# Kernel optimization log

Measured on AMD Instinct MI355X. Metric: run time of the kernel, lower is better.

## Reference

```python
import jax, jax.numpy as jnp
import numpy as np

T_STEPS = 100
T_EMB = 16
EPS = 1e-8


def sin_emb(t, dim):
    # sinusoidal_time_embedding: [cos(t*f), sin(t*f)] with f = exp(-log(1e4)*i/half)
    half = dim // 2
    freqs = jnp.exp(-jnp.log(jnp.float32(10000.0)) * jnp.arange(half, dtype=jnp.float32) / half)
    a = t.astype(jnp.float32)[:, None] * freqs[None, :]
    return jnp.concatenate([jnp.cos(a), jnp.sin(a)], axis=-1)


def lstm_layer(x_tbf, W_ih, W_hh, b):
    # x_tbf: [T, B, F]; torch gate order i, f, g, o
    B = x_tbf.shape[1]
    H = W_hh.shape[1]

    def step(carry, x_t):
        h, c = carry
        g = x_t @ W_ih.T + h @ W_hh.T + b
        i, f, gg, o = jnp.split(g, 4, axis=-1)
        c = jax.nn.sigmoid(f) * c + jax.nn.sigmoid(i) * jnp.tanh(gg)
        h = jax.nn.sigmoid(o) * jnp.tanh(c)
        return (h, c), h

    z = jnp.zeros((B, H), x_tbf.dtype)
    (h, c), ys = jax.lax.scan(step, (z, z), x_tbf)
    return ys, h


def _forward(x_hist, x_future, y0, turb_idx, pred_steps, init_noise, turb_emb,
             W_ih0, W_hh0, b_ih0, b_hh0, W_ih1, W_hh1, b_ih1, b_hh1,
             W1, b1, W2, b2, W3, b3):
    betas = jnp.linspace(1e-4, 0.02, T_STEPS).astype(jnp.float32)
    alphas = 1.0 - betas
    alpha_bars = jnp.cumprod(alphas)

    B = x_hist.shape[0]
    emb = turb_emb[turb_idx]  # [B, E]
    eh = jnp.broadcast_to(emb[:, None, :], (B, x_hist.shape[1], emb.shape[1]))
    ef = jnp.broadcast_to(emb[:, None, :], (B, x_future.shape[1], emb.shape[1]))
    xh = jnp.concatenate([x_hist, eh], axis=-1).transpose(1, 0, 2)    # [T_in, B, F+E]
    xf = jnp.concatenate([x_future, ef], axis=-1).transpose(1, 0, 2)  # [P, B, exo+E]

    ys0, _ = lstm_layer(xh, W_ih0, W_hh0, b_ih0 + b_hh0)
    _, enc_out = lstm_layer(ys0, W_ih1, W_hh1, b_ih1 + b_hh1)         # [B, H] = h[-1]

    def mlp(x):
        h = jax.nn.relu(x @ W1.T + b1)
        h = jax.nn.relu(h @ W2.T + b2)
        return h @ W3.T + b3

    def ar_step(prev_y, xs):
        exo_t, step, y_init = xs
        cond = jnp.concatenate([enc_out, exo_t, prev_y], axis=1)  # [B, cond_dim]
        h_e = sin_emb(jnp.full((B,), step), T_EMB)

        def dstep(y, t):
            t_e = sin_emb(jnp.full((B,), t), T_EMB)
            eps_hat = mlp(jnp.concatenate([cond, y, t_e, h_e], axis=1))  # [B,1]
            b_t, a_t, ab_t = betas[t], alphas[t], alpha_bars[t]
            pred_x0 = (y - jnp.sqrt(1.0 - ab_t) * eps_hat) / (jnp.sqrt(ab_t) + EPS)
            mean = (y - b_t / (jnp.sqrt(1.0 - ab_t) + EPS) * eps_hat) / (jnp.sqrt(a_t) + EPS)
            # eval mode -> deterministic sampling: posterior noise term is zero
            return jnp.where(t == 0, pred_x0, mean), None

        y, _ = jax.lax.scan(dstep, y_init, jnp.arange(T_STEPS - 1, -1, -1))
        return y, y[:, 0]

    _, seq = jax.lax.scan(ar_step, y0, (xf, jnp.arange(pred_steps), init_noise))
    return seq.T[:, :, None]  # [B, pred_steps, 1]


def setup_inputs() -> dict:
    key = jax.random.key(0)
    ks = list(jax.random.split(key, 24))
    kit = iter(ks)
    B, T_IN, F_IN, EXO, EMB, PRED, HID, NTURB = 1024, 96, 8, 6, 16, 8, 128, 100
    in0 = F_IN + EMB                 # 24
    cond_dim = HID + EXO + EMB + 1   # 151
    in_mlp = cond_dim + 1 + T_EMB + T_EMB  # 184

    def nrm(shape, s=0.05):
        return jax.random.normal(next(kit), shape, jnp.float32) * s

    return {
        'x_hist': jax.random.normal(next(kit), (B, T_IN, F_IN), jnp.float32),
        'x_future': jax.random.normal(next(kit), (B, PRED, EXO), jnp.float32),
        'y0': jnp.zeros((B, 1), jnp.float32),
        'turb_idx': jax.random.randint(next(kit), (B,), 0, NTURB),
        'pred_steps': PRED,
        'init_noise': jax.random.normal(next(kit), (PRED, B, 1), jnp.float32),
        'turb_emb': nrm((NTURB, EMB), 0.1),
        'W_ih0': nrm((4 * HID, in0)), 'W_hh0': nrm((4 * HID, HID)),
        'b_ih0': jnp.zeros((4 * HID,), jnp.float32), 'b_hh0': jnp.zeros((4 * HID,), jnp.float32),
        'W_ih1': nrm((4 * HID, HID)), 'W_hh1': nrm((4 * HID, HID)),
        'b_ih1': jnp.zeros((4 * HID,), jnp.float32), 'b_hh1': jnp.zeros((4 * HID,), jnp.float32),
        'W1': nrm((HID, in_mlp)), 'b1': jnp.zeros((HID,), jnp.float32),
        'W2': nrm((HID, HID)), 'b2': jnp.zeros((HID,), jnp.float32),
        'W3': nrm((1, HID)), 'b3': jnp.zeros((1,), jnp.float32),
    }


def reference(x_hist, x_future, y0, turb_idx, pred_steps, init_noise, turb_emb,
              W_ih0, W_hh0, b_ih0, b_hh0, W_ih1, W_hh1, b_ih1, b_hh1,
              W1, b1, W2, b2, W3, b3):
    return _forward(x_hist, x_future, y0, turb_idx, pred_steps, init_noise, turb_emb,
                    W_ih0, W_hh0, b_ih0, b_hh0, W_ih1, W_hh1, b_ih1, b_hh1,
                    W1, b1, W2, b2, W3, b3)
```

## Files before the change

kernel.cpp:

```cpp
#include <hip/hip_runtime.h>
#include <hip/hip_fp16.h>
#include <stdint.h>


typedef __attribute__((ext_vector_type(2))) _Float16 half2_t;
typedef __attribute__((ext_vector_type(8))) _Float16 v8h;
typedef __attribute__((ext_vector_type(4))) float v4f;

#define DEV __device__ __forceinline__

DEV uint32_t pack2f(float a, float b) {
  __half ha = __float2half_rn(a), hb = __float2half_rn(b);
  return (uint32_t)__half_as_ushort(ha) | ((uint32_t)__half_as_ushort(hb) << 16);
}

DEV float2 up2(uint32_t u) {
  half2_t h = __builtin_bit_cast(half2_t, u);
  return make_float2((float)h.x, (float)h.y);
}

DEV float fast_ex2(float x) {
#if __has_builtin(__builtin_amdgcn_exp2f)
  return __builtin_amdgcn_exp2f(x);
#else
  return exp2f(x);
#endif
}
DEV float fast_rcp(float x) {
#if __has_builtin(__builtin_amdgcn_rcpf)
  return __builtin_amdgcn_rcpf(x);
#else
  return 1.f / x;
#endif
}
DEV float sigm(float x) { return fast_rcp(1.f + fast_ex2(-1.4426950408889634f * x)); }
DEV float tanh_f(float x) {
  return 2.f * fast_rcp(1.f + fast_ex2(-2.8853900817779268f * x)) - 1.f;
}

DEV uint32_t pk_add(uint32_t a, uint32_t b) {
  return __builtin_bit_cast(uint32_t,
      __builtin_bit_cast(half2_t, a) + __builtin_bit_cast(half2_t, b));
}

DEV uint32_t pk_relufma(uint32_t w, uint32_t y, uint32_t b) {
  half2_t r = __builtin_bit_cast(half2_t, w) * __builtin_bit_cast(half2_t, y) +
              __builtin_bit_cast(half2_t, b);
  half2_t z = {(_Float16)0.f, (_Float16)0.f};
#if __has_builtin(__builtin_elementwise_max)
  r = __builtin_elementwise_max(r, z);
#else
  uint32_t u = __builtin_bit_cast(uint32_t, r);
  uint32_t mask = ((u >> 15) & 1u) * 0xFFFFu | ((u >> 31) & 1u) * 0xFFFF0000u;
  r = __builtin_bit_cast(half2_t, u & ~mask);
#endif
  return __builtin_bit_cast(uint32_t, r);
}

DEV uint32_t cvtpk(float y) {
#if __has_builtin(__builtin_amdgcn_cvt_pkrtz)
  return __builtin_bit_cast(uint32_t, __builtin_amdgcn_cvt_pkrtz(y, y));
#else
  return pack2f(y, y);
#endif
}

DEV float rowsum16(float v) {
  int x;
  x = __builtin_amdgcn_update_dpp(0, __builtin_bit_cast(int, v), 0x111, 0xf, 0xf, true);
  v += __builtin_bit_cast(float, x);
  x = __builtin_amdgcn_update_dpp(0, __builtin_bit_cast(int, v), 0x112, 0xf, 0xf, true);
  v += __builtin_bit_cast(float, x);
  x = __builtin_amdgcn_update_dpp(0, __builtin_bit_cast(int, v), 0x114, 0xf, 0xf, true);
  v += __builtin_bit_cast(float, x);
  x = __builtin_amdgcn_update_dpp(0, __builtin_bit_cast(int, v), 0x118, 0xf, 0xf, true);
  v += __builtin_bit_cast(float, x);
  return v;
}

static constexpr size_t OFF_XH  = 0;
static constexpr size_t OFF_W0  = 4718592;
static constexpr size_t OFF_BS0 = 4882432;
static constexpr size_t OFF_W1L = 4884480;
static constexpr size_t OFF_BS1 = 5146624;
static constexpr size_t OFF_W2P = 5148672;
static constexpr size_t OFF_ENC = 5181440;
static constexpr size_t OFF_YS0 = 5705728;

__global__ void k_prep_xh(const float* __restrict__ xh, const int* __restrict__ tix,
                          const float* __restrict__ temb, uint32_t* __restrict__ out) {
  int idx = blockIdx.x * 256 + threadIdx.x;
  if (idx >= 96 * 1024 * 12) return;
  int m = idx % 12;
  int tb = idx / 12;
  int b = tb & 1023, t = tb >> 10;
  int k0 = 2 * m, k1 = k0 + 1;
  float v0 = (k0 < 8) ? xh[(b * 96 + t) * 8 + k0] : temb[tix[b] * 16 + (k0 - 8)];
  float v1 = (k1 < 8) ? xh[(b * 96 + t) * 8 + k1] : temb[tix[b] * 16 + (k1 - 8)];
  out[idx] = pack2f(v0, v1);
}

__global__ void k_prep_w(const float* __restrict__ Wih0, const float* __restrict__ Whh0,
                         const float* __restrict__ bih0, const float* __restrict__ bhh0,
                         const float* __restrict__ Wih1, const float* __restrict__ Whh1,
                         const float* __restrict__ bih1, const float* __restrict__ bhh1,
                         const float* __restrict__ W2,
                         uint32_t* __restrict__ w0p, uint32_t* __restrict__ w1p,
                         uint32_t* __restrict__ w2p, float* __restrict__ bs0,
                         float* __restrict__ bs1) {
  int idx = blockIdx.x * 256 + threadIdx.x;
  if (idx < 40960) {
    int w = idx / 5120;
    int r = idx % 5120;
    int T = r / 1280; r %= 1280;
    int f = r / 256;  r %= 256;
    int l = r >> 2, c = r & 3;
    int m = l & 15, qf = l >> 4;
    int g = (m & 3) * 128 + w * 16 + (m >> 2) * 4 + T;
    int k0 = f * 32 + qf * 8 + 2 * c, k1 = k0 + 1;
    float a = (k0 < 24) ? Wih0[g * 24 + k0] : ((k0 < 152) ? Whh0[g * 128 + k0 - 24] : 0.f);
    float b = (k1 < 24) ? Wih0[g * 24 + k1] : ((k1 < 152) ? Whh0[g * 128 + k1 - 24] : 0.f);
    w0p[idx] = pack2f(a, b);
  } else if (idx < 106496) {
    int i = idx - 40960;
    int w = i / 8192;
    int r = i % 8192;
    int T = r / 2048; r %= 2048;
    int f = r / 256;  r %= 256;
    int l = r >> 2, c = r & 3;
    int m = l & 15, qf = l >> 4;
    int g = (m & 3) * 128 + w * 16 + (m >> 2) * 4 + T;
    int k0 = f * 32 + qf * 8 + 2 * c, k1 = k0 + 1;
    float a = (k0 < 128) ? Wih1[g * 128 + k0] : Whh1[g * 128 + k0 - 128];
    float b = (k1 < 128) ? Wih1[g * 128 + k1] : Whh1[g * 128 + k1 - 128];
    w1p[i] = pack2f(a, b);
  } else if (idx < 114688) {
    int i = idx - 106496;
    w2p[i] = pack2f(W2[2 * i], W2[2 * i + 1]);
  } else if (idx < 115200) {
    int i = idx - 114688;
    bs0[i] = bih0[i] + bhh0[i];
  } else if (idx < 115712) {
    int i = idx - 115200;
    bs1[i] = bih1[i] + bhh1[i];
  }
}

__global__ __launch_bounds__(512, 2) void k_lstm0(const uint32_t* __restrict__ xh16,
                                                  const uint32_t* __restrict__ w0A,
                                                  const float* __restrict__ bs0,
                                                  __half* __restrict__ ys0) {
  __shared__ __align__(16) __half inb[2][16][160];
  const int tid = threadIdx.x;
  const int w = tid >> 6, l = tid & 63;
  const int n = l & 15, ql = l >> 4;
  const int ju = w * 16 + ql * 4;
  const int bbase = blockIdx.x * 16;

  uint4 Af[4][5];
#pragma unroll
  for (int T = 0; T < 4; T++)
#pragma unroll
    for (int f = 0; f < 5; f++)
      Af[T][f] = ((const uint4*)w0A)[((w * 4 + T) * 5 + f) * 64 + l];
  float bias[4][4];
#pragma unroll
  for (int T = 0; T < 4; T++)
#pragma unroll
    for (int r = 0; r < 4; r++) bias[T][r] = bs0[r * 128 + ju + T];

  for (int i = tid; i < 2560; i += 512) ((uint32_t*)inb)[i] = 0u;
  __syncthreads();
  if (tid < 192) {
    int b = tid / 12, m = tid % 12;
    ((uint32_t*)&inb[0][b][0])[m] = xh16[(0 * 1024 + bbase + b) * 12 + m];
  }
  float cst[4] = {0.f, 0.f, 0.f, 0.f};
  __syncthreads();

  for (int t = 0; t < 96; t++) {
    const int cur = t & 1, nxt = cur ^ 1;
    uint32_t sx = 0;
    int sb = 0, sm = 0;
    if (t < 95 && tid < 192) {
      sb = tid / 12; sm = tid % 12;
      sx = xh16[((t + 1) * 1024 + bbase + sb) * 12 + sm];
    }
    v4f acc[4];
#pragma unroll
    for (int T = 0; T < 4; T++) acc[T] = (v4f){0.f, 0.f, 0.f, 0.f};
#pragma unroll
    for (int f = 0; f < 5; f++) {
      uint4 bu = *(const uint4*)&inb[cur][n][f * 32 + ql * 8];
      v8h Bv = __builtin_bit_cast(v8h, bu);
#pragma unroll
      for (int T = 0; T < 4; T++)
        acc[T] = __builtin_amdgcn_mfma_f32_16x16x32_f16(
            __builtin_bit_cast(v8h, Af[T][f]), Bv, acc[T], 0, 0, 0);
    }
    float hv[4];
#pragma unroll
    for (int T = 0; T < 4; T++) {
      float gi = acc[T][0] + bias[T][0];
      float gf = acc[T][1] + bias[T][1];
      float gg = acc[T][2] + bias[T][2];
      float go = acc[T][3] + bias[T][3];
      float c = sigm(gf) * cst[T] + sigm(gi) * tanh_f(gg);
      cst[T] = c;
      hv[T] = sigm(go) * tanh_f(c);
    }
    uint32_t h01 = pack2f(hv[0], hv[1]), h23 = pack2f(hv[2], hv[3]);
    *(uint2*)&inb[nxt][n][24 + ju] = make_uint2(h01, h23);
    *(uint2*)((__half*)ys0 + (size_t)(t * 1024 + bbase + n) * 128 + ju) = make_uint2(h01, h23);
    if (t < 95 && tid < 192) ((uint32_t*)&inb[nxt][sb][0])[sm] = sx;
    __syncthreads();
  }
}

__global__ __launch_bounds__(512, 2) void k_lstm1(const uint32_t* __restrict__ ys0u,
                                                  const uint32_t* __restrict__ w1A,
                                                  const float* __restrict__ bs1,
                                                  float* __restrict__ enc) {
  __shared__ __align__(16) __half inb[2][16][264];
  const int tid = threadIdx.x;
  const int w = tid >> 6, l = tid & 63;
  const int n = l & 15, ql = l >> 4;
  const int ju = w * 16 + ql * 4;
  const int bbase = blockIdx.x * 16;
  const int sb = tid >> 5, sc = tid & 31;

  uint4 Af[4][8];
#pragma unroll
  for (int T = 0; T < 4; T++)
#pragma unroll
    for (int f = 0; f < 8; f++)
      Af[T][f] = ((const uint4*)w1A)[((w * 4 + T) * 8 + f) * 64 + l];
  float bias[4][4];
#pragma unroll
  for (int T = 0; T < 4; T++)
#pragma unroll
    for (int r = 0; r < 4; r++) bias[T][r] = bs1[r * 128 + ju + T];

  for (int i = tid; i < 4224; i += 512) ((uint32_t*)inb)[i] = 0u;
  __syncthreads();
  {
    uint2 v = ((const uint2*)ys0u)[(size_t)(0 * 1024 + bbase + sb) * 32 + sc];
    *(uint2*)&inb[0][sb][sc * 4] = v;
  }
  float cst[4] = {0.f, 0.f, 0.f, 0.f};
  __syncthreads();

  for (int t = 0; t < 96; t++) {
    const int cur = t & 1, nxt = cur ^ 1;
    uint2 sv = make_uint2(0u, 0u);
    if (t < 95)
      sv = ((const uint2*)ys0u)[(size_t)((t + 1) * 1024 + bbase + sb) * 32 + sc];
    v4f acc[4];
#pragma unroll
    for (int T = 0; T < 4; T++) acc[T] = (v4f){0.f, 0.f, 0.f, 0.f};
#pragma unroll
    for (int f = 0; f < 8; f++) {
      uint4 bu = *(const uint4*)&inb[cur][n][f * 32 + ql * 8];
      v8h Bv = __builtin_bit_cast(v8h, bu);
#pragma unroll
      for (int T = 0; T < 4; T++)
        acc[T] = __builtin_amdgcn_mfma_f32_16x16x32_f16(
            __builtin_bit_cast(v8h, Af[T][f]), Bv, acc[T], 0, 0, 0);
    }
    float hv[4];
#pragma unroll
    for (int T = 0; T < 4; T++) {
      float gi = acc[T][0] + bias[T][0];
      float gf = acc[T][1] + bias[T][1];
      float gg = acc[T][2] + bias[T][2];
      float go = acc[T][3] + bias[T][3];
      float c = sigm(gf) * cst[T] + sigm(gi) * tanh_f(gg);
      cst[T] = c;
      hv[T] = sigm(go) * tanh_f(c);
    }
    *(uint2*)&inb[nxt][n][128 + ju] = make_uint2(pack2f(hv[0], hv[1]), pack2f(hv[2], hv[3]));
    if (t < 95) *(uint2*)&inb[nxt][sb][sc * 4] = sv;
    if (t == 95)
      *(float4*)&enc[(size_t)(bbase + n) * 128 + ju] = make_float4(hv[0], hv[1], hv[2], hv[3]);
    __syncthreads();
  }
}

__global__ __launch_bounds__(256, 1) void k_diff(
    const float* __restrict__ xfut, const float* __restrict__ y0,
    const int* __restrict__ tix, const float* __restrict__ noise,
    const float* __restrict__ temb, const float* __restrict__ W1,
    const float* __restrict__ b1, const float* __restrict__ b2,
    const float* __restrict__ W3, const float* __restrict__ b3,
    const uint32_t* __restrict__ w2p, const float* __restrict__ enc,
    float* __restrict__ out) {
  __shared__ uint32_t W1sL[128 * 65];
  __shared__ uint32_t W1xL[128 * 29];
  __shared__ uint32_t encPL[16 * 65];
  __shared__ uint32_t embPL[16 * 9];
  __shared__ float teL[100][16];
  __shared__ float2 ccL[100];
  __shared__ __align__(16) __half tprojL[100 * 128];
  __shared__ __half hprojL[8 * 128];
  __shared__ __align__(16) float partL[2][4][16];
  __shared__ uint32_t encdL[256 * 17];

  const int tid = threadIdx.x;
  const int w = tid >> 6, l = tid & 63;
  const int m = l & 15, q = l >> 4;
  const int bbase = blockIdx.x * 16;

  for (int i = tid; i < 128 * 64; i += 256) {
    int r = i >> 6, c = i & 63;
    W1sL[r * 65 + c] = pack2f(W1[r * 184 + 2 * c], W1[r * 184 + 2 * c + 1]);
  }
  for (int i = tid; i < 128 * 28; i += 256) {
    int r = i / 28, c = i % 28;
    W1xL[r * 29 + c] = pack2f(W1[r * 184 + 128 + 2 * c], W1[r * 184 + 129 + 2 * c]);
  }
  for (int i = tid; i < 16 * 64; i += 256) {
    int bb = i >> 6, c = i & 63;
    encPL[bb * 65 + c] = pack2f(enc[(bbase + bb) * 128 + 2 * c],
                                enc[(bbase + bb) * 128 + 2 * c + 1]);
  }
  for (int i = tid; i < 16 * 8; i += 256) {
    int bb = i >> 3, c = i & 7;
    const float* er = temb + tix[bbase + bb] * 16;
    embPL[bb * 9 + c] = pack2f(er[2 * c], er[2 * c + 1]);
  }
  for (int p = tid; p < 1600; p += 256) {
    int tt = p >> 4, i = p & 15;
    float f = expf(-logf(10000.f) * (float)(i & 7) / 8.f);
    float a = (float)tt * f;
    teL[tt][i] = (i < 8) ? cosf(a) : sinf(a);
  }
  for (int qq = tid; qq < 100; qq += 256) {
    float ab = 1.f, beta = 0.f;
    for (int i = 0; i <= qq; i++) {
      beta = 1e-4f + (0.02f - 1e-4f) * (float)i / 99.f;
      ab *= (1.f - beta);
    }
    float cs, cd;
    if (qq == 0) { cs = sqrtf(1.f - ab); cd = 1.f / (sqrtf(ab) + 1e-8f); }
    else { cs = beta / (sqrtf(1.f - ab) + 1e-8f); cd = 1.f / (sqrtf(1.f - beta) + 1e-8f); }
    ccL[qq] = make_float2(cs, cd);
  }
  __syncthreads();

  {
    int k = tid & 127, hs = tid >> 7;
    float wte[16], whe[16];
#pragma unroll
    for (int i = 0; i < 8; i++) {
      float2 a = up2(W1xL[k * 29 + 12 + i]);
      wte[2 * i] = a.x; wte[2 * i + 1] = a.y;
      float2 bqq = up2(W1xL[k * 29 + 20 + i]);
      whe[2 * i] = bqq.x; whe[2 * i + 1] = bqq.y;
    }
    for (int tt = hs * 50; tt < hs * 50 + 50; tt++) {
      float s = 0.f;
#pragma unroll
      for (int i = 0; i < 16; i++) s += wte[i] * teL[tt][i];
      tprojL[tt * 128 + k] = __float2half_rn(s);
    }
    if (hs == 0) {
      for (int ss = 0; ss < 8; ss++) {
        float s = 0.f;
#pragma unroll
        for (int i = 0; i < 16; i++) s += whe[i] * teL[ss][i];
        hprojL[ss * 128 + k] = __float2half_rn(s);
      }
    }
  }

  for (int pi = 0; pi < 16; pi++) {
    int k0 = (pi >> 2) * 32 + q * 8 + (pi & 3) * 2;
    half2_t a0 = {(_Float16)0.f, (_Float16)0.f};
    half2_t a1 = a0;
    const uint32_t* wr0 = &W1sL[k0 * 65];
    const uint32_t* wr1 = &W1sL[(k0 + 1) * 65];
    const uint32_t* ep = &encPL[m * 65];
#pragma unroll 8
    for (int c = 0; c < 64; c++) {
      half2_t e = __builtin_bit_cast(half2_t, ep[c]);
      a0 += __builtin_bit_cast(half2_t, wr0[c]) * e;
      a1 += __builtin_bit_cast(half2_t, wr1[c]) * e;
    }
#pragma unroll
    for (int c = 0; c < 8; c++) {
      half2_t e = __builtin_bit_cast(half2_t, embPL[m * 9 + c]);
      a0 += __builtin_bit_cast(half2_t, W1xL[k0 * 29 + 3 + c]) * e;
      a1 += __builtin_bit_cast(half2_t, W1xL[(k0 + 1) * 29 + 3 + c]) * e;
    }
    float e0 = b1[k0] + (float)a0.x + (float)a0.y;
    float e1 = b1[k0 + 1] + (float)a1.x + (float)a1.y;
    encdL[tid * 17 + pi] = pack2f(e0, e1);
  }

  uint4 Bf[2][4];
  const uint4* w2u4 = (const uint4*)w2p;
#pragma unroll
  for (int tt = 0; tt < 2; tt++) {
    int n = w * 32 + tt * 16 + m;
#pragma unroll
    for (int f = 0; f < 4; f++) Bf[tt][f] = w2u4[n * 16 + f * 4 + q];
  }
  const float w3v0 = W3[w * 32 + m], w3v1 = W3[w * 32 + 16 + m];
  const float b2v0 = b2[w * 32 + m], b2v1 = b2[w * 32 + 16 + m];
  const float b3v = b3[0];

  uint32_t w1yP[16];
#pragma unroll
  for (int pi = 0; pi < 16; pi++) {
    int k0 = (pi >> 2) * 32 + q * 8 + (pi & 3) * 2;
    uint32_t ua = W1xL[k0 * 29 + 11];
    uint32_t ub = W1xL[(k0 + 1) * 29 + 11];
    w1yP[pi] = (ua >> 16) | (ub & 0xFFFF0000u);
  }

  float prev_y = y0[bbase + m];
  float noi[8];
#pragma unroll
  for (int s = 0; s < 8; s++) noi[s] = noise[s * 1024 + bbase + m];
  __syncthreads();

  int buf = 0;
  for (int s = 0; s < 8; s++) {
    float xf[6];
#pragma unroll
    for (int i = 0; i < 6; i++) xf[i] = xfut[((bbase + m) * 8 + s) * 6 + i];
    uint32_t bph[16];
#pragma unroll
    for (int pi = 0; pi < 16; pi++) {
      int k0 = (pi >> 2) * 32 + q * 8 + (pi & 3) * 2;
      float2 ed = up2(encdL[tid * 17 + pi]);
      float e0 = ed.x, e1 = ed.y;
#pragma unroll
      for (int c = 0; c < 3; c++) {
        float2 w0v = up2(W1xL[k0 * 29 + c]);
        float2 w1v = up2(W1xL[(k0 + 1) * 29 + c]);
        e0 += w0v.x * xf[2 * c] + w0v.y * xf[2 * c + 1];
        e1 += w1v.x * xf[2 * c] + w1v.y * xf[2 * c + 1];
      }
      e0 += up2(W1xL[k0 * 29 + 11]).x * prev_y;
      e1 += up2(W1xL[(k0 + 1) * 29 + 11]).x * prev_y;
      e0 += (float)hprojL[s * 128 + k0];
      e1 += (float)hprojL[s * 128 + k0 + 1];
      bph[pi] = pack2f(e0, e1);
    }

    float y = noi[s];
    uint32_t bt[16];
    {
      const uint4* tb = (const uint4*)(tprojL + 99 * 128 + q * 8);
      uint4 t0 = tb[0], t1 = tb[4], t2 = tb[8], t3 = tb[12];
      bt[0] = pk_add(bph[0], t0.x);  bt[1] = pk_add(bph[1], t0.y);
      bt[2] = pk_add(bph[2], t0.z);  bt[3] = pk_add(bph[3], t0.w);
      bt[4] = pk_add(bph[4], t1.x);  bt[5] = pk_add(bph[5], t1.y);
      bt[6] = pk_add(bph[6], t1.z);  bt[7] = pk_add(bph[7], t1.w);
      bt[8] = pk_add(bph[8], t2.x);  bt[9] = pk_add(bph[9], t2.y);
      bt[10] = pk_add(bph[10], t2.z); bt[11] = pk_add(bph[11], t2.w);
      bt[12] = pk_add(bph[12], t3.x); bt[13] = pk_add(bph[13], t3.y);
      bt[14] = pk_add(bph[14], t3.z); bt[15] = pk_add(bph[15], t3.w);
    }
    float2 ccv = ccL[99];

    for (int t = 99; t >= 0; t--) {
      uint32_t yP = cvtpk(y);
      v4f c0a = {0.f, 0.f, 0.f, 0.f}, c0b = c0a, c1a = c0a, c1b = c0a;
#pragma unroll
      for (int f = 0; f < 4; f++) {
        uint4 au;
        au.x = pk_relufma(w1yP[4 * f + 0], yP, bt[4 * f + 0]);
        au.y = pk_relufma(w1yP[4 * f + 1], yP, bt[4 * f + 1]);
        au.z = pk_relufma(w1yP[4 * f + 2], yP, bt[4 * f + 2]);
        au.w = pk_relufma(w1yP[4 * f + 3], yP, bt[4 * f + 3]);
        v8h A = __builtin_bit_cast(v8h, au);
        if (f & 1) {
          c0b = __builtin_amdgcn_mfma_f32_16x16x32_f16(A, __builtin_bit_cast(v8h, Bf[0][f]), c0b, 0, 0, 0);
          c1b = __builtin_amdgcn_mfma_f32_16x16x32_f16(A, __builtin_bit_cast(v8h, Bf[1][f]), c1b, 0, 0, 0);
        } else {
          c0a = __builtin_amdgcn_mfma_f32_16x16x32_f16(A, __builtin_bit_cast(v8h, Bf[0][f]), c0a, 0, 0, 0);
          c1a = __builtin_amdgcn_mfma_f32_16x16x32_f16(A, __builtin_bit_cast(v8h, Bf[1][f]), c1a, 0, 0, 0);
        }
      }
      const int tn = (t > 0) ? t - 1 : 0;
      const uint4* tb = (const uint4*)(tprojL + tn * 128 + q * 8);
      uint4 t0 = tb[0], t1 = tb[4], t2 = tb[8], t3 = tb[12];
      float2 ccn = ccL[tn];
      v4f c0 = c0a + c0b, c1 = c1a + c1b;
      float pr[4];
#pragma unroll
      for (int r = 0; r < 4; r++) {
        pr[r] = fmaxf(c0[r] + b2v0, 0.f) * w3v0 + fmaxf(c1[r] + b2v1, 0.f) * w3v1;
        pr[r] = rowsum16(pr[r]);
      }
      if ((l & 15) == 15)
        *(float4*)&partL[buf][w][q * 4] = make_float4(pr[0], pr[1], pr[2], pr[3]);
      uint32_t btn[16];
      btn[0] = pk_add(bph[0], t0.x);  btn[1] = pk_add(bph[1], t0.y);
      btn[2] = pk_add(bph[2], t0.z);  btn[3] = pk_add(bph[3], t0.w);
      btn[4] = pk_add(bph[4], t1.x);  btn[5] = pk_add(bph[5], t1.y);
      btn[6] = pk_add(bph[6], t1.z);  btn[7] = pk_add(bph[7], t1.w);
      btn[8] = pk_add(bph[8], t2.x);  btn[9] = pk_add(bph[9], t2.y);
      btn[10] = pk_add(bph[10], t2.z); btn[11] = pk_add(bph[11], t2.w);
      btn[12] = pk_add(bph[12], t3.x); btn[13] = pk_add(bph[13], t3.y);
      btn[14] = pk_add(bph[14], t3.z); btn[15] = pk_add(bph[15], t3.w);
      __syncthreads();
      float eps = b3v + ((partL[buf][0][m] + partL[buf][1][m]) +
                         (partL[buf][2][m] + partL[buf][3][m]));
      y = (y - ccv.x * eps) * ccv.y;
      ccv = ccn;
#pragma unroll
      for (int pi = 0; pi < 16; pi++) bt[pi] = btn[pi];
      buf ^= 1;
    }
    if (w == 0 && l < 16) out[(bbase + l) * 8 + s] = y;
    prev_y = y;
  }
}

extern "C" void kernel_launch(void* const* d_in, const int* in_sizes, int n_in,
                              void* d_out, int out_size, void* d_ws, size_t ws_size,
                              hipStream_t stream) {
  const float* x_hist    = (const float*)d_in[0];
  const float* x_future  = (const float*)d_in[1];
  const float* y0        = (const float*)d_in[2];
  const int*   turb_idx  = (const int*)d_in[3];
  const float* init_noise = (const float*)d_in[5];
  const float* turb_emb  = (const float*)d_in[6];
  const float* W_ih0     = (const float*)d_in[7];
  const float* W_hh0     = (const float*)d_in[8];
  const float* b_ih0     = (const float*)d_in[9];
  const float* b_hh0     = (const float*)d_in[10];
  const float* W_ih1     = (const float*)d_in[11];
  const float* W_hh1     = (const float*)d_in[12];
  const float* b_ih1     = (const float*)d_in[13];
  const float* b_hh1     = (const float*)d_in[14];
  const float* W1        = (const float*)d_in[15];
  const float* b1        = (const float*)d_in[16];
  const float* W2        = (const float*)d_in[17];
  const float* b2        = (const float*)d_in[18];
  const float* W3        = (const float*)d_in[19];
  const float* b3        = (const float*)d_in[20];

  char* ws = (char*)d_ws;
  uint32_t* xh16 = (uint32_t*)(ws + OFF_XH);
  uint32_t* w0p  = (uint32_t*)(ws + OFF_W0);
  float*    bs0  = (float*)(ws + OFF_BS0);
  uint32_t* w1p  = (uint32_t*)(ws + OFF_W1L);
  float*    bs1  = (float*)(ws + OFF_BS1);
  uint32_t* w2p  = (uint32_t*)(ws + OFF_W2P);
  float*    encf = (float*)(ws + OFF_ENC);
  __half*   ys0h = (__half*)(ws + OFF_YS0);

  k_prep_xh<<<4608, 256, 0, stream>>>(x_hist, turb_idx, turb_emb, xh16);
  k_prep_w<<<452, 256, 0, stream>>>(W_ih0, W_hh0, b_ih0, b_hh0,
                                    W_ih1, W_hh1, b_ih1, b_hh1,
                                    W2, w0p, w1p, w2p, bs0, bs1);
  k_lstm0<<<64, 512, 0, stream>>>(xh16, w0p, bs0, ys0h);
  k_lstm1<<<64, 512, 0, stream>>>((const uint32_t*)ys0h, w1p, bs1, encf);
  k_diff<<<64, 256, 0, stream>>>(x_future, y0, turb_idx, init_noise, turb_emb,
                                 W1, b1, b2, W3, b3, w2p, encf, (float*)d_out);
}
```

Before: 675.7 us.

## Process two 16-row batch chunks per diffusion block and use lighter LDS barriers

The diffusion kernel now handles 32 batch rows per block as two interleaved 16-row chains, halving the grid to 32 blocks. Each denoising step issues independent MFMA chains for both chunks, so one chunk's dependency latency can be hidden behind the other's work, and the per-step barrier cost is spread over twice the rows. The LSTM and diffusion barriers are replaced by an inline s_waitcnt lgkmcnt(0) plus s_barrier that waits only on LDS traffic. In exchange, fewer CUs are used, register pressure roughly doubles in the diffusion loop, and the weight-staging prologue is repeated over fewer blocks but each block does more of it.

After: 928.1 us. 37.4% more time.

```diff
diff --git a/kernel.cpp b/kernel.cpp
--- a/kernel.cpp
+++ b/kernel.cpp
@@ -8,6 +8,10 @@
 typedef __attribute__((ext_vector_type(4))) float v4f;
 
 #define DEV __device__ __forceinline__
+
+DEV void barrier_lds() {
+  asm volatile("s_waitcnt lgkmcnt(0)\ns_barrier" ::: "memory");
+}
 
 DEV uint32_t pack2f(float a, float b) {
   __half ha = __float2half_rn(a), hb = __float2half_rn(b);
@@ -213,7 +217,7 @@
     *(uint2*)&inb[nxt][n][24 + ju] = make_uint2(h01, h23);
     *(uint2*)((__half*)ys0 + (size_t)(t * 1024 + bbase + n) * 128 + ju) = make_uint2(h01, h23);
     if (t < 95 && tid < 192) ((uint32_t*)&inb[nxt][sb][0])[sm] = sx;
-    __syncthreads();
+    barrier_lds();
   }
 }
 
@@ -282,7 +286,7 @@
     if (t < 95) *(uint2*)&inb[nxt][sb][sc * 4] = sv;
     if (t == 95)
       *(float4*)&enc[(size_t)(bbase + n) * 128 + ju] = make_float4(hv[0], hv[1], hv[2], hv[3]);
-    __syncthreads();
+    barrier_lds();
   }
 }
 
@@ -296,19 +300,19 @@
     float* __restrict__ out) {
   __shared__ uint32_t W1sL[128 * 65];
   __shared__ uint32_t W1xL[128 * 29];
-  __shared__ uint32_t encPL[16 * 65];
-  __shared__ uint32_t embPL[16 * 9];
+  __shared__ uint32_t encPL[32 * 65];
+  __shared__ uint32_t embPL[32 * 9];
   __shared__ float teL[100][16];
   __shared__ float2 ccL[100];
   __shared__ __align__(16) __half tprojL[100 * 128];
   __shared__ __half hprojL[8 * 128];
-  __shared__ __align__(16) float partL[2][4][16];
-  __shared__ uint32_t encdL[256 * 17];
+  __shared__ __align__(16) float partL[2][2][4][16];
+  __shared__ uint32_t encdL[2][256 * 17];
 
   const int tid = threadIdx.x;
   const int w = tid >> 6, l = tid & 63;
   const int m = l & 15, q = l >> 4;
-  const int bbase = blockIdx.x * 16;
+  const int bbase = blockIdx.x * 32;
 
   for (int i = tid; i < 128 * 64; i += 256) {
     int r = i >> 6, c = i & 63;
@@ -318,12 +322,12 @@
     int r = i / 28, c = i % 28;
     W1xL[r * 29 + c] = pack2f(W1[r * 184 + 128 + 2 * c], W1[r * 184 + 129 + 2 * c]);
   }
-  for (int i = tid; i < 16 * 64; i += 256) {
+  for (int i = tid; i < 32 * 64; i += 256) {
     int bb = i >> 6, c = i & 63;
     encPL[bb * 65 + c] = pack2f(enc[(bbase + bb) * 128 + 2 * c],
                                 enc[(bbase + bb) * 128 + 2 * c + 1]);
   }
-  for (int i = tid; i < 16 * 8; i += 256) {
+  for (int i = tid; i < 32 * 8; i += 256) {
     int bb = i >> 3, c = i & 7;
     const float* er = temb + tix[bbase + bb] * 16;
     embPL[bb * 9 + c] = pack2f(er[2 * c], er[2 * c + 1]);
@@ -373,28 +377,31 @@
     }
   }
 
-  for (int pi = 0; pi < 16; pi++) {
-    int k0 = (pi >> 2) * 32 + q * 8 + (pi & 3) * 2;
-    half2_t a0 = {(_Float16)0.f, (_Float16)0.f};
-    half2_t a1 = a0;
-    const uint32_t* wr0 = &W1sL[k0 * 65];
-    const uint32_t* wr1 = &W1sL[(k0 + 1) * 65];
-    const uint32_t* ep = &encPL[m * 65];
+#pragma unroll
+  for (int ch = 0; ch < 2; ch++) {
+    for (int pi = 0; pi < 16; pi++) {
+      int k0 = (pi >> 2) * 32 + q * 8 + (pi & 3) * 2;
+      half2_t a0 = {(_Float16)0.f, (_Float16)0.f};
+      half2_t a1 = a0;
+      const uint32_t* wr0 = &W1sL[k0 * 65];
+      const uint32_t* wr1 = &W1sL[(k0 + 1) * 65];
+      const uint32_t* ep = &encPL[(ch * 16 + m) * 65];
 #pragma unroll 8
-    for (int c = 0; c < 64; c++) {
-      half2_t e = __builtin_bit_cast(half2_t, ep[c]);
-      a0 += __builtin_bit_cast(half2_t, wr0[c]) * e;
-      a1 += __builtin_bit_cast(half2_t, wr1[c]) * e;
-    }
-#pragma unroll
-    for (int c = 0; c < 8; c++) {
-      half2_t e = __builtin_bit_cast(half2_t, embPL[m * 9 + c]);
-      a0 += __builtin_bit_cast(half2_t, W1xL[k0 * 29 + 3 + c]) * e;
-      a1 += __builtin_bit_cast(half2_t, W1xL[(k0 + 1) * 29 + 3 + c]) * e;
-    }
-    float e0 = b1[k0] + (float)a0.x + (float)a0.y;
-    float e1 = b1[k0 + 1] + (float)a1.x + (float)a1.y;
-    encdL[tid * 17 + pi] = pack2f(e0, e1);
+      for (int c = 0; c < 64; c++) {
+        half2_t e = __builtin_bit_cast(half2_t, ep[c]);
+        a0 += __builtin_bit_cast(half2_t, wr0[c]) * e;
+        a1 += __builtin_bit_cast(half2_t, wr1[c]) * e;
+      }
+#pragma unroll
+      for (int c = 0; c < 8; c++) {
+        half2_t e = __builtin_bit_cast(half2_t, embPL[(ch * 16 + m) * 9 + c]);
+        a0 += __builtin_bit_cast(half2_t, W1xL[k0 * 29 + 3 + c]) * e;
+        a1 += __builtin_bit_cast(half2_t, W1xL[(k0 + 1) * 29 + 3 + c]) * e;
+      }
+      float e0 = b1[k0] + (float)a0.x + (float)a0.y;
+      float e1 = b1[k0 + 1] + (float)a1.x + (float)a1.y;
+      encdL[ch][tid * 17 + pi] = pack2f(e0, e1);
+    }
   }
 
   uint4 Bf[2][4];
@@ -418,105 +425,121 @@
     w1yP[pi] = (ua >> 16) | (ub & 0xFFFF0000u);
   }
 
-  float prev_y = y0[bbase + m];
-  float noi[8];
-#pragma unroll
-  for (int s = 0; s < 8; s++) noi[s] = noise[s * 1024 + bbase + m];
+  float py0 = y0[bbase + m], py1 = y0[bbase + 16 + m];
   __syncthreads();
 
   int buf = 0;
   for (int s = 0; s < 8; s++) {
-    float xf[6];
-#pragma unroll
-    for (int i = 0; i < 6; i++) xf[i] = xfut[((bbase + m) * 8 + s) * 6 + i];
-    uint32_t bph[16];
+    float xf0[6], xf1[6];
+#pragma unroll
+    for (int i = 0; i < 6; i++) {
+      xf0[i] = xfut[((bbase + m) * 8 + s) * 6 + i];
+      xf1[i] = xfut[((bbase + 16 + m) * 8 + s) * 6 + i];
+    }
+    uint32_t bph0[16], bph1[16];
 #pragma unroll
     for (int pi = 0; pi < 16; pi++) {
       int k0 = (pi >> 2) * 32 + q * 8 + (pi & 3) * 2;
-      float2 ed = up2(encdL[tid * 17 + pi]);
-      float e0 = ed.x, e1 = ed.y;
+      float2 ed0 = up2(encdL[0][tid * 17 + pi]);
+      float2 ed1 = up2(encdL[1][tid * 17 + pi]);
+      float e00 = ed0.x, e01 = ed0.y, e10 = ed1.x, e11 = ed1.y;
 #pragma unroll
       for (int c = 0; c < 3; c++) {
         float2 w0v = up2(W1xL[k0 * 29 + c]);
         float2 w1v = up2(W1xL[(k0 + 1) * 29 + c]);
-        e0 += w0v.x * xf[2 * c] + w0v.y * xf[2 * c + 1];
-        e1 += w1v.x * xf[2 * c] + w1v.y * xf[2 * c + 1];
-      }
-      e0 += up2(W1xL[k0 * 29 + 11]).x * prev_y;
-      e1 += up2(W1xL[(k0 + 1) * 29 + 11]).x * prev_y;
-      e0 += (float)hprojL[s * 128 + k0];
-      e1 += (float)hprojL[s * 128 + k0 + 1];
-      bph[pi] = pack2f(e0, e1);
-    }
-
-    float y = noi[s];
-    uint32_t bt[16];
+        e00 += w0v.x * xf0[2 * c] + w0v.y * xf0[2 * c + 1];
+        e01 += w1v.x * xf0[2 * c] + w1v.y * xf0[2 * c + 1];
+        e10 += w0v.x * xf1[2 * c] + w0v.y * xf1[2 * c + 1];
+        e11 += w1v.x * xf1[2 * c] + w1v.y * xf1[2 * c + 1];
+      }
+      float wp0 = up2(W1xL[k0 * 29 + 11]).x;
+      float wp1 = up2(W1xL[(k0 + 1) * 29 + 11]).x;
+      e00 += wp0 * py0;  e01 += wp1 * py0;
+      e10 += wp0 * py1;  e11 += wp1 * py1;
+      float hp0 = (float)hprojL[s * 128 + k0];
+      float hp1 = (float)hprojL[s * 128 + k0 + 1];
+      bph0[pi] = pack2f(e00 + hp0, e01 + hp1);
+      bph1[pi] = pack2f(e10 + hp0, e11 + hp1);
+    }
+
+    float ya = noise[s * 1024 + bbase + m];
+    float yb = noise[s * 1024 + bbase + 16 + m];
+    uint32_t bt0[16], bt1[16];
     {
       const uint4* tb = (const uint4*)(tprojL + 99 * 128 + q * 8);
       uint4 t0 = tb[0], t1 = tb[4], t2 = tb[8], t3 = tb[12];
-      bt[0] = pk_add(bph[0], t0.x);  bt[1] = pk_add(bph[1], t0.y);
-      bt[2] = pk_add(bph[2], t0.z);  bt[3] = pk_add(bph[3], t0.w);
-      bt[4] = pk_add(bph[4], t1.x);  bt[5] = pk_add(bph[5], t1.y);
-      bt[6] = pk_add(bph[6], t1.z);  bt[7] = pk_add(bph[7], t1.w);
-      bt[8] = pk_add(bph[8], t2.x);  bt[9] = pk_add(bph[9], t2.y);
-      bt[10] = pk_add(bph[10], t2.z); bt[11] = pk_add(bph[11], t2.w);
-      bt[12] = pk_add(bph[12], t3.x); bt[13] = pk_add(bph[13], t3.y);
-      bt[14] = pk_add(bph[14], t3.z); bt[15] = pk_add(bph[15], t3.w);
+      uint32_t tv[16] = {t0.x, t0.y, t0.z, t0.w, t1.x, t1.y, t1.z, t1.w,
+                         t2.x, t2.y, t2.z, t2.w, t3.x, t3.y, t3.z, t3.w};
+#pragma unroll
+      for (int pi = 0; pi < 16; pi++) {
+        bt0[pi] = pk_add(bph0[pi], tv[pi]);
+        bt1[pi] = pk_add(bph1[pi], tv[pi]);
+      }
     }
     float2 ccv = ccL[99];
 
     for (int t = 99; t >= 0; t--) {
-      uint32_t yP = cvtpk(y);
-      v4f c0a = {0.f, 0.f, 0.f, 0.f}, c0b = c0a, c1a = c0a, c1b = c0a;
+      uint32_t yPa = cvtpk(ya), yPb = cvtpk(yb);
+      v4f d00 = {0.f, 0.f, 0.f, 0.f}, d01 = d00, d10 = d00, d11 = d00;
 #pragma unroll
       for (int f = 0; f < 4; f++) {
         uint4 au;
-        au.x = pk_relufma(w1yP[4 * f + 0], yP, bt[4 * f + 0]);
-        au.y = pk_relufma(w1yP[4 * f + 1], yP, bt[4 * f + 1]);
-        au.z = pk_relufma(w1yP[4 * f + 2], yP, bt[4 * f + 2]);
-        au.w = pk_relufma(w1yP[4 * f + 3], yP, bt[4 * f + 3]);
+        au.x = pk_relufma(w1yP[4 * f + 0], yPa, bt0[4 * f + 0]);
+        au.y = pk_relufma(w1yP[4 * f + 1], yPa, bt0[4 * f + 1]);
+        au.z = pk_relufma(w1yP[4 * f + 2], yPa, bt0[4 * f + 2]);
+        au.w = pk_relufma(w1yP[4 * f + 3], yPa, bt0[4 * f + 3]);
         v8h A = __builtin_bit_cast(v8h, au);
-        if (f & 1) {
-          c0b = __builtin_amdgcn_mfma_f32_16x16x32_f16(A, __builtin_bit_cast(v8h, Bf[0][f]), c0b, 0, 0, 0);
-          c1b = __builtin_amdgcn_mfma_f32_16x16x32_f16(A, __builtin_bit_cast(v8h, Bf[1][f]), c1b, 0, 0, 0);
-        } else {
-          c0a = __builtin_amdgcn_mfma_f32_16x16x32_f16(A, __builtin_bit_cast(v8h, Bf[0][f]), c0a, 0, 0, 0);
-          c1a = __builtin_amdgcn_mfma_f32_16x16x32_f16(A, __builtin_bit_cast(v8h, Bf[1][f]), c1a, 0, 0, 0);
-        }
+        d00 = __builtin_amdgcn_mfma_f32_16x16x32_f16(A, __builtin_bit_cast(v8h, Bf[0][f]), d00, 0, 0, 0);
+        d01 = __builtin_amdgcn_mfma_f32_16x16x32_f16(A, __builtin_bit_cast(v8h, Bf[1][f]), d01, 0, 0, 0);
+        uint4 av;
+        av.x = pk_relufma(w1yP[4 * f + 0], yPb, bt1[4 * f + 0]);
+        av.y = pk_relufma(w1yP[4 * f + 1], yPb, bt1[4 * f + 1]);
+        av.z = pk_relufma(w1yP[4 * f + 2], yPb, bt1[4 * f + 2]);
+        av.w = pk_relufma(w1yP[4 * f + 3], yPb, bt1[4 * f + 3]);
+        v8h Ab = __builtin_bit_cast(v8h, av);
+        d10 = __builtin_amdgcn_mfma_f32_16x16x32_f16(Ab, __builtin_bit_cast(v8h, Bf[0][f]), d10, 0, 0, 0);
+        d11 = __builtin_amdgcn_mfma_f32_16x16x32_f16(Ab, __builtin_bit_cast(v8h, Bf[1][f]), d11, 0, 0, 0);
       }
       const int tn = (t > 0) ? t - 1 : 0;
       const uint4* tb = (const uint4*)(tprojL + tn * 128 + q * 8);
       uint4 t0 = tb[0], t1 = tb[4], t2 = tb[8], t3 = tb[12];
       float2 ccn = ccL[tn];
-      v4f c0 = c0a + c0b, c1 = c1a + c1b;
-      float pr[4];
+      float pra[4], prb[4];
 #pragma unroll
       for (int r = 0; r < 4; r++) {
-        pr[r] = fmaxf(c0[r] + b2v0, 0.f) * w3v0 + fmaxf(c1[r] + b2v1, 0.f) * w3v1;
-        pr[r] = rowsum16(pr[r]);
-      }
-      if ((l & 15) == 15)
-        *(float4*)&partL[buf][w][q * 4] = make_float4(pr[0], pr[1], pr[2], pr[3]);
-      uint32_t btn[16];
-      btn[0] = pk_add(bph[0], t0.x);  btn[1] = pk_add(bph[1], t0.y);
-      btn[2] = pk_add(bph[2], t0.z);  btn[3] = pk_add(bph[3], t0.w);
-      btn[4] = pk_add(bph[4], t1.x);  btn[5] = pk_add(bph[5], t1.y);
-      btn[6] = pk_add(bph[6], t1.z);  btn[7] = pk_add(bph[7], t1.w);
-      btn[8] = pk_add(bph[8], t2.x);  btn[9] = pk_add(bph[9], t2.y);
-      btn[10] = pk_add(bph[10], t2.z); btn[11] = pk_add(bph[11], t2.w);
-      btn[12] = pk_add(bph[12], t3.x); btn[13] = pk_add(bph[13], t3.y);
-      btn[14] = pk_add(bph[14], t3.z); btn[15] = pk_add(bph[15], t3.w);
-      __syncthreads();
-      float eps = b3v + ((partL[buf][0][m] + partL[buf][1][m]) +
-                         (partL[buf][2][m] + partL[buf][3][m]));
-      y = (y - ccv.x * eps) * ccv.y;
+        pra[r] = fmaxf(d00[r] + b2v0, 0.f) * w3v0 + fmaxf(d01[r] + b2v1, 0.f) * w3v1;
+        pra[r] = rowsum16(pra[r]);
+        prb[r] = fmaxf(d10[r] + b2v0, 0.f) * w3v0 + fmaxf(d11[r] + b2v1, 0.f) * w3v1;
+        prb[r] = rowsum16(prb[r]);
+      }
+      if ((l & 15) == 15) {
+        *(float4*)&partL[0][buf][w][q * 4] = make_float4(pra[0], pra[1], pra[2], pra[3]);
+        *(float4*)&partL[1][buf][w][q * 4] = make_float4(prb[0], prb[1], prb[2], prb[3]);
+      }
+      uint32_t tv[16] = {t0.x, t0.y, t0.z, t0.w, t1.x, t1.y, t1.z, t1.w,
+                         t2.x, t2.y, t2.z, t2.w, t3.x, t3.y, t3.z, t3.w};
+      uint32_t btn0[16], btn1[16];
+#pragma unroll
+      for (int pi = 0; pi < 16; pi++) {
+        btn0[pi] = pk_add(bph0[pi], tv[pi]);
+        btn1[pi] = pk_add(bph1[pi], tv[pi]);
+      }
+      barrier_lds();
+      float eps0 = b3v + ((partL[0][buf][0][m] + partL[0][buf][1][m]) +
+                          (partL[0][buf][2][m] + partL[0][buf][3][m]));
+      float eps1 = b3v + ((partL[1][buf][0][m] + partL[1][buf][1][m]) +
+                          (partL[1][buf][2][m] + partL[1][buf][3][m]));
+      ya = (ya - ccv.x * eps0) * ccv.y;
+      yb = (yb - ccv.x * eps1) * ccv.y;
       ccv = ccn;
 #pragma unroll
-      for (int pi = 0; pi < 16; pi++) bt[pi] = btn[pi];
+      for (int pi = 0; pi < 16; pi++) { bt0[pi] = btn0[pi]; bt1[pi] = btn1[pi]; }
       buf ^= 1;
     }
-    if (w == 0 && l < 16) out[(bbase + l) * 8 + s] = y;
-    prev_y = y;
+    if (w == 0 && l < 16) out[(bbase + l) * 8 + s] = ya;
+    if (w == 1 && l < 16) out[(bbase + 16 + l) * 8 + s] = yb;
+    py0 = ya;
+    py1 = yb;
   }
 }
 
@@ -560,6 +583,6 @@
                                     W2, w0p, w1p, w2p, bs0, bs1);
   k_lstm0<<<64, 512, 0, stream>>>(xh16, w0p, bs0, ys0h);
   k_lstm1<<<64, 512, 0, stream>>>((const uint32_t*)ys0h, w1p, bs1, encf);
-  k_diff<<<64, 256, 0, stream>>>(x_future, y0, turb_idx, init_noise, turb_emb,
+  k_diff<<<32, 256, 0, stream>>>(x_future, y0, turb_idx, init_noise, turb_emb,
                                  W1, b1, b2, W3, b3, w2p, encf, (float*)d_out);
 }
```
